# Optimization experiments

Hardware: AMD Instinct MI355X
Metric: run time of the kernel (lower is better)

Reference implementation:

```python
import math
import jax, jax.numpy as jnp
import numpy as np

B, S, D_MODEL, H = 2, 2048, 1024, 16
HD = D_MODEL // H  # head_dim = 64


def setup_inputs() -> dict:
    key = jax.random.key(0)
    ks = jax.random.split(key, 5)
    scale = 1.0 / math.sqrt(D_MODEL)
    return {
        "x": jax.random.normal(ks[0], (B, S, D_MODEL), dtype=jnp.float32),
        "attention_mask": jnp.ones((B, S), dtype=jnp.int32),
        "causal": 1,
        "Wq": jax.random.normal(ks[1], (D_MODEL, D_MODEL), dtype=jnp.float32) * scale,
        "Wk": jax.random.normal(ks[2], (D_MODEL, D_MODEL), dtype=jnp.float32) * scale,
        "Wv": jax.random.normal(ks[3], (D_MODEL, D_MODEL), dtype=jnp.float32) * scale,
        "Wo": jax.random.normal(ks[4], (D_MODEL, D_MODEL), dtype=jnp.float32) * scale,
    }


def reference(x, attention_mask, causal, Wq, Wk, Wv, Wo):
    b, s, d = x.shape
    # QKV projections, split heads -> (b, h, s, hd)
    q = (x @ Wq).reshape(b, s, H, HD).transpose(0, 2, 1, 3)
    k = (x @ Wk).reshape(b, s, H, HD).transpose(0, 2, 1, 3)
    v = (x @ Wv).reshape(b, s, H, HD).transpose(0, 2, 1, 3)

    score = jnp.einsum("bhqd,bhkd->bhqk", q, k) / math.sqrt(HD)

    neg_inf = jnp.float32(-jnp.inf)
    if causal:
        causal_mask = jnp.tril(jnp.ones((s, s), dtype=bool))  # (s, s)
        score = jnp.where(causal_mask[None, None, :, :], score, neg_inf)
    key_mask = attention_mask.astype(bool)[:, None, None, :]  # (b,1,1,s)
    score = jnp.where(key_mask, score, neg_inf)

    attn = jax.nn.softmax(score, axis=-1)  # numerically stable (max-subtracted)
    out = jnp.einsum("bhqk,bhkd->bhqd", attn, v)  # (b,h,s,hd)
    out = out.transpose(0, 2, 1, 3).reshape(b, s, d)
    return out @ Wo
```

## Files before the change

kernel.cpp:

```cpp
#include <hip/hip_runtime.h>
#include <hip/hip_bf16.h>

#define B_  2
#define S_  2048
#define D_  1024
#define H_  16
#define HD_ 64
#define BS_ (B_*S_)

typedef __attribute__((ext_vector_type(8))) short bf16x8;
typedef __attribute__((ext_vector_type(4))) float f32x4;
typedef __attribute__((ext_vector_type(4))) float float4v;
typedef __attribute__((ext_vector_type(4))) unsigned short ushort4v;
typedef __attribute__((ext_vector_type(2))) unsigned int uint2v;

__device__ __forceinline__ unsigned short f2bf(float f) {
  union { float f; unsigned int u; } v; v.f = f;
  unsigned int u = v.u;
  return (unsigned short)((u + 0x7fffu + ((u >> 16) & 1u)) >> 16);
}
__device__ __forceinline__ float bf2f(unsigned short u) {
  union { unsigned int i; float f; } v; v.i = ((unsigned int)u) << 16; return v.f;
}
__device__ __forceinline__ unsigned int cvtpk(float lo, float hi) {
  unsigned int r;
  asm("v_cvt_pk_bf16_f32 %0, %1, %2" : "=v"(r) : "v"(lo), "v"(hi));
  return r;
}

__device__ __forceinline__ void plswap16(float& a, float& b) {
#if __has_builtin(__builtin_amdgcn_permlane16_swap)
  uint2v r = __builtin_amdgcn_permlane16_swap(__float_as_uint(a), __float_as_uint(b), false, false);
  a = __uint_as_float(r[0]); b = __uint_as_float(r[1]);
#else
  asm volatile("v_permlane16_swap_b32 %0, %1" : "+v"(a), "+v"(b));
#endif
}
__device__ __forceinline__ void plswap32(float& a, float& b) {
#if __has_builtin(__builtin_amdgcn_permlane32_swap)
  uint2v r = __builtin_amdgcn_permlane32_swap(__float_as_uint(a), __float_as_uint(b), false, false);
  a = __uint_as_float(r[0]); b = __uint_as_float(r[1]);
#else
  asm volatile("v_permlane32_swap_b32 %0, %1" : "+v"(a), "+v"(b));
#endif
}
__device__ __forceinline__ float wave_max_lg(float x) {
  float t;
  asm volatile("v_mov_b32 %0, %1" : "=v"(t) : "v"(x));
  plswap16(x, t); x = fmaxf(x, t);
  asm volatile("v_mov_b32 %0, %1" : "=v"(t) : "v"(x));
  plswap32(x, t); x = fmaxf(x, t);
  return x;
}
__device__ __forceinline__ float wave_sum_lg(float x) {
  float t;
  asm volatile("v_mov_b32 %0, %1" : "=v"(t) : "v"(x));
  plswap16(x, t); x += t;
  asm volatile("v_mov_b32 %0, %1" : "=v"(t) : "v"(x));
  plswap32(x, t); x += t;
  return x;
}

__device__ __forceinline__ void gload16(const void* g, void* l) {
  __builtin_amdgcn_global_load_lds((const __attribute__((address_space(1))) void*)g,
                                   (__attribute__((address_space(3))) void*)l, 16, 0, 0);
}

__device__ __forceinline__ f32x4 mfma16(bf16x8 a, bf16x8 b, f32x4 c) {
  return __builtin_amdgcn_mfma_f32_16x16x32_bf16(a, b, c, 0, 0, 0);
}

__global__ __launch_bounds__(256) void k_prep(const float* __restrict__ x, unsigned short* __restrict__ xb,
                                              const float* __restrict__ w0, const float* __restrict__ w1,
                                              const float* __restrict__ w2, const float* __restrict__ w3,
                                              unsigned short* __restrict__ o0, unsigned short* __restrict__ o1,
                                              unsigned short* __restrict__ o2, unsigned short* __restrict__ o3) {
  const int bid = blockIdx.x;
  if (bid < 2048) {
    int i = bid * 256 + threadIdx.x;
    float4v a = ((const float4v*)x)[2*i];
    float4v b = ((const float4v*)x)[2*i + 1];
    union { bf16x8 v; unsigned short u[8]; } o;
#pragma unroll
    for (int j = 0; j < 4; ++j) { o.u[j] = f2bf(a[j]); o.u[4+j] = f2bf(b[j]); }
    ((bf16x8*)xb)[i] = o.v;
    return;
  }
  const int wid = bid - 2048;
  const int xx = wid & 15, yy = (wid >> 4) & 15, zz = wid >> 8;
  const float* w = zz == 0 ? w0 : zz == 1 ? w1 : zz == 2 ? w2 : w3;
  unsigned short* o = zz == 0 ? o0 : zz == 1 ? o1 : zz == 2 ? o2 : o3;
  __shared__ unsigned short til[64][68];
  const int n0 = xx * 64, k0 = yy * 64;
  const int t = threadIdx.x, r = t >> 4, c4 = t & 15;
#pragma unroll
  for (int i = 0; i < 4; ++i) {
    float4v v = *(const float4v*)(w + (size_t)(k0 + i*16 + r) * D_ + n0 + c4*4);
#pragma unroll
    for (int j = 0; j < 4; ++j) til[i*16 + r][c4*4 + j] = f2bf(v[j]);
  }
  __syncthreads();
#pragma unroll
  for (int i = 0; i < 4; ++i) {
    ushort4v u;
#pragma unroll
    for (int j = 0; j < 4; ++j) u[j] = til[c4*4 + j][i*16 + r];
    *(ushort4v*)(o + (size_t)(n0 + i*16 + r) * D_ + k0 + c4*4) = u;
  }
}

template <int MODE, typename OutT>
__device__ __forceinline__ void gemm_body(const unsigned short* __restrict__ A,
                                          const unsigned short* __restrict__ Bt,
                                          OutT* __restrict__ C,
                                          int M, int N, int K, int mblk, int nblk) {
  __shared__ unsigned short As[128 * 64];
  __shared__ unsigned short Bs[128 * 64];
  const int tid = threadIdx.x;
  const int w = tid >> 6, lane = tid & 63;
  const int lg = lane >> 4, li = lane & 15;
  const int m0 = mblk * 128, n0 = nblk * 128;
  const int wr = (w >> 1) * 64, wc = (w & 1) * 64;
  f32x4 acc[4][4] = {};
  for (int kt = 0; kt < K; kt += 64) {
#pragma unroll
    for (int i = 0; i < 4; ++i) {
      int c = (i*4 + w) * 64 + lane;
      int r = c >> 3, kc = c & 7;
      int off = ((kc ^ (r & 7)) << 3);
      gload16(A  + (size_t)(m0 + r) * K + kt + off, (char*)As + (i*4 + w) * 1024);
      gload16(Bt + (size_t)(n0 + r) * K + kt + off, (char*)Bs + (i*4 + w) * 1024);
    }
    __syncthreads();
#pragma unroll
    for (int ks = 0; ks < 2; ++ks) {
      bf16x8 af[4], bfr[4];
#pragma unroll
      for (int m = 0; m < 4; ++m) {
        int rr = wr + m*16 + li;
        int ch = (ks*4 + lg) ^ (rr & 7);
        af[m] = *(const bf16x8*)((const char*)As + rr*128 + ch*16);
      }
#pragma unroll
      for (int n = 0; n < 4; ++n) {
        int rr = wc + n*16 + li;
        int ch = (ks*4 + lg) ^ (rr & 7);
        bfr[n] = *(const bf16x8*)((const char*)Bs + rr*128 + ch*16);
      }
#pragma unroll
      for (int m = 0; m < 4; ++m)
#pragma unroll
        for (int n = 0; n < 4; ++n)
          acc[m][n] = mfma16(af[m], bfr[n], acc[m][n]);
    }
    __syncthreads();
  }
#pragma unroll
  for (int m = 0; m < 4; ++m)
#pragma unroll
    for (int n = 0; n < 4; ++n) {
      if (MODE == 2) {
        int gr = m0 + wr + m*16 + lg*4;
        int gc = n0 + wc + n*16 + li;
        int bb = gr >> 11, ss = gr & 2047, hh = gc >> 6, dd = gc & 63;
        unsigned short* p = (unsigned short*)C + ((size_t)((bb*H_ + hh)*HD_ + dd)) * S_ + ss;
        uint2v o2;
        o2[0] = cvtpk(acc[m][n][0], acc[m][n][1]);
        o2[1] = cvtpk(acc[m][n][2], acc[m][n][3]);
        *(uint2v*)p = o2;
      } else {
#pragma unroll
        for (int j = 0; j < 4; ++j) {
          int row = m0 + wr + m*16 + lg*4 + j;
          int col = n0 + wc + n*16 + li;
          if (MODE == 1) ((float*)C)[(size_t)row * N + col] = acc[m][n][j];
          else ((unsigned short*)C)[(size_t)row * N + col] = f2bf(acc[m][n][j]);
        }
      }
    }
}

__global__ __launch_bounds__(256, 2) void k_qkv(const unsigned short* __restrict__ xb,
    const unsigned short* __restrict__ wqt, const unsigned short* __restrict__ wkt,
    const unsigned short* __restrict__ wvt,
    unsigned short* __restrict__ Qb, unsigned short* __restrict__ Kb, unsigned short* __restrict__ Vtb) {
  const int z = blockIdx.z;
  if (z == 2) {
    gemm_body<2, unsigned short>(xb, wvt, Vtb, BS_, D_, D_, blockIdx.x, blockIdx.y);
  } else {
    gemm_body<0, unsigned short>(xb, z ? wkt : wqt, z ? Kb : Qb, BS_, D_, D_, blockIdx.x, blockIdx.y);
  }
}

__global__ __launch_bounds__(256, 2) void k_out(const unsigned short* __restrict__ AO,
                                                const unsigned short* __restrict__ wot,
                                                float* __restrict__ out) {
  gemm_body<1, float>(AO, wot, out, BS_, D_, D_, blockIdx.x, blockIdx.y);
}

__global__ __launch_bounds__(128, 2) void k_attn(const unsigned short* __restrict__ Q,
                                                 const unsigned short* __restrict__ K,
                                                 const unsigned short* __restrict__ Vt,
                                                 unsigned short* __restrict__ AO) {
  __shared__ unsigned short Ks[2 * 64 * 64];
  __shared__ unsigned short Vs[2 * 64 * 64];
  __shared__ unsigned short Ps[2 * 16 * 64];
  const int bh = blockIdx.x;
  const int qb = 63 - blockIdx.y;
  const int nkt = (qb >> 1) + 1;
  const int b = bh >> 4, h = bh & 15;
  const int tid = threadIdx.x, w = tid >> 6, lane = tid & 63;
  const int lg = lane >> 4, li = lane & 15;
  unsigned short* Psw = Ps + w * 1024;
  const float SC2 = 0.18033688f;

  const int qglob = qb*32 + w*16 + li;
  const unsigned short* qptr = Q + (size_t)(b*S_ + qglob) * D_ + h*HD_;
  union { bf16x8 v; unsigned short u[8]; } q0u, q1u;
  q0u.v = *(const bf16x8*)(qptr + lg*8);
  q1u.v = *(const bf16x8*)(qptr + 32 + lg*8);
#pragma unroll
  for (int j = 0; j < 8; ++j) {
    q0u.u[j] = f2bf(bf2f(q0u.u[j]) * SC2);
    q1u.u[j] = f2bf(bf2f(q1u.u[j]) * SC2);
  }
  const bf16x8 qf0 = q0u.v, qf1 = q1u.v;

  int paddr[8];
#pragma unroll
  for (int kj = 0; kj < 4; ++kj)
#pragma unroll
    for (int hh = 0; hh < 2; ++hh)
      paddr[kj*2 + hh] = li*128 + (((2*kj + (lg >> 1)) ^ (li & 7)) << 4) + (lg & 1)*8 + 4*hh;
  int pboff[2];
#pragma unroll
  for (int ks = 0; ks < 2; ++ks)
    pboff[ks] = li*128 + (((ks*4 + lg) ^ (li & 7)) << 4);

  int kofs[4], vofs[4];
#pragma unroll
  for (int i = 0; i < 4; ++i) {
    int c = i*128 + tid;
    int r = c >> 3, kc = c & 7;
    int off = ((kc ^ (r & 7)) << 3);
    kofs[i] = r * D_ + off;
    vofs[i] = r * S_ + off;
  }
  const unsigned short* kg = K  + (size_t)(b*S_) * D_ + h*HD_;
  const unsigned short* vg = Vt + (size_t)bh * HD_ * S_;

  f32x4 oacc[4] = {};
  float mrow = -1e30f, lrow = 0.f;

  auto stage = [&](int bsel, const unsigned short* kp, const unsigned short* vp) {
    char* KsB = (char*)Ks + bsel * 8192;
    char* VsB = (char*)Vs + bsel * 8192;
#pragma unroll
    for (int i = 0; i < 4; ++i) {
      gload16(kp + kofs[i], KsB + (i*2 + w) * 1024);
      gload16(vp + vofs[i], VsB + (i*2 + w) * 1024);
    }
  };

  stage(0, kg, vg);
  __syncthreads();

  for (int kt = 0; kt < nkt; ++kt) {
    const int cur = kt & 1;
    if (kt + 1 < nkt) {
      kg += 64 * D_; vg += 64;
      stage(cur ^ 1, kg, vg);
    }
    const char* KsB = (const char*)Ks + cur * 8192;
    const char* VsB = (const char*)Vs + cur * 8192;

    f32x4 sc[4];
    __builtin_amdgcn_s_setprio(1);
#pragma unroll
    for (int kj = 0; kj < 4; ++kj) {
      f32x4 t = {};
      t = mfma16(*(const bf16x8*)(KsB + kj*2048 + pboff[0]), qf0, t);
      t = mfma16(*(const bf16x8*)(KsB + kj*2048 + pboff[1]), qf1, t);
      sc[kj] = t;
    }
    __builtin_amdgcn_s_setprio(0);

    if (kt == nkt - 1) {
      const int qrel = qglob - kt*64;
#pragma unroll
      for (int kj = 0; kj < 4; ++kj)
#pragma unroll
        for (int j = 0; j < 4; ++j)
          if (kj*16 + lg*4 + j > qrel) sc[kj][j] = -1e30f;
    }

    float mx = sc[0][0];
#pragma unroll
    for (int kj = 0; kj < 4; ++kj)
#pragma unroll
      for (int j = 0; j < 4; ++j) mx = fmaxf(mx, sc[kj][j]);
    mx = wave_max_lg(mx);
    if (__any(mx > mrow + 8.f)) {
      const float mnew = fmaxf(mrow, mx);
      const float alpha = exp2f(mrow - mnew);
#pragma unroll
      for (int n = 0; n < 4; ++n)
#pragma unroll
        for (int j = 0; j < 4; ++j) oacc[n][j] *= alpha;
      lrow *= alpha;
      mrow = mnew;
    }
    f32x4 pv[4];
    float rs = 0.f;
#pragma unroll
    for (int kj = 0; kj < 4; ++kj)
#pragma unroll
      for (int j = 0; j < 4; ++j) {
        float p = exp2f(sc[kj][j] - mrow);
        rs += p;
        pv[kj][j] = p;
      }
    lrow += rs;

#pragma unroll
    for (int kj = 0; kj < 4; ++kj) {
      *(unsigned int*)((char*)Psw + paddr[kj*2 + 0]) = cvtpk(pv[kj][0], pv[kj][1]);
      *(unsigned int*)((char*)Psw + paddr[kj*2 + 1]) = cvtpk(pv[kj][2], pv[kj][3]);
    }

    const bf16x8 pf0 = *(const bf16x8*)((const char*)Psw + pboff[0]);
    const bf16x8 pf1 = *(const bf16x8*)((const char*)Psw + pboff[1]);
    __builtin_amdgcn_s_setprio(1);
#pragma unroll
    for (int n = 0; n < 4; ++n) {
      int vr = n*16 + li;
      int ch0 = lg ^ (vr & 7), ch1 = (4 + lg) ^ (vr & 7);
      oacc[n] = mfma16(*(const bf16x8*)(VsB + vr*128 + ch0*16), pf0, oacc[n]);
      oacc[n] = mfma16(*(const bf16x8*)(VsB + vr*128 + ch1*16), pf1, oacc[n]);
    }
    __builtin_amdgcn_s_setprio(0);
    __syncthreads();
  }

  lrow = wave_sum_lg(lrow);
  const float inv = 1.0f / lrow;
  unsigned short* aorow = AO + (size_t)(b*S_ + qglob) * D_ + h*HD_;
#pragma unroll
  for (int n = 0; n < 4; ++n) {
    uint2v o2;
    o2[0] = cvtpk(oacc[n][0] * inv, oacc[n][1] * inv);
    o2[1] = cvtpk(oacc[n][2] * inv, oacc[n][3] * inv);
    *(uint2v*)(aorow + n*16 + lg*4) = o2;
  }
}

extern "C" void kernel_launch(void* const* d_in, const int* in_sizes, int n_in,
                              void* d_out, int out_size, void* d_ws, size_t ws_size,
                              hipStream_t stream) {
  const float* x  = (const float*)d_in[0];
  const float* Wq = (const float*)d_in[3];
  const float* Wk = (const float*)d_in[4];
  const float* Wv = (const float*)d_in[5];
  const float* Wo = (const float*)d_in[6];
  float* out = (float*)d_out;

  unsigned short* ws  = (unsigned short*)d_ws;
  unsigned short* xb  = ws;
  unsigned short* wqt = xb  + (size_t)BS_ * D_;
  unsigned short* wkt = wqt + (size_t)D_ * D_;
  unsigned short* wvt = wkt + (size_t)D_ * D_;
  unsigned short* wot = wvt + (size_t)D_ * D_;
  unsigned short* Qb  = wot + (size_t)D_ * D_;
  unsigned short* Kb  = Qb  + (size_t)BS_ * D_;
  unsigned short* Vtb = Kb  + (size_t)BS_ * D_;
  unsigned short* AO  = Vtb + (size_t)BS_ * D_;

  k_prep<<<3072, 256, 0, stream>>>(x, xb, Wq, Wk, Wv, Wo, wqt, wkt, wvt, wot);
  k_qkv<<<dim3(32, 8, 3), 256, 0, stream>>>(xb, wqt, wkt, wvt, Qb, Kb, Vtb);
  k_attn<<<dim3(32, 64), 128, 0, stream>>>(Qb, Kb, Vtb, AO);
  k_out<<<dim3(32, 8), 256, 0, stream>>>(AO, wot, out);
}
```

Before: 117.9 us.

## Split long causal attention query blocks across two KV halves with combine kernel

Attention blocks now cover 64 query rows with 4 waves (256 threads), and the 16 longest query blocks per head are split into two KV-range chunks whose partial outputs and max/sum stats go to scratch buffers that reuse the xb/weight workspace. A new combine kernel merges the two partials with a log-sum-exp rescale. A constant lookup table orders the work longest-first to balance the causal load. The cost is an extra launch, extra global traffic for partials, and a combine kernel containing redundant leftover code.

```diff
diff --git a/kernel.cpp b/kernel.cpp
--- a/kernel.cpp
+++ b/kernel.cpp
@@ -13,6 +13,13 @@
 typedef __attribute__((ext_vector_type(4))) float float4v;
 typedef __attribute__((ext_vector_type(4))) unsigned short ushort4v;
 typedef __attribute__((ext_vector_type(2))) unsigned int uint2v;
+
+__constant__ unsigned char TQ[48] = {31,31,30,15, 30,29,29,28,14, 28,27,27,26,13,
+                                     26,25,25,24,12, 24,23,23,22,11, 22,21,21,20,10,
+                                     20,19,19,18,9, 18,17,17,16,8, 16,7, 6,5,4,3,2,1,0};
+__constant__ unsigned char TH[48] = {0,1,1,2, 0,0,1,1,2, 0,0,1,1,2,
+                                     0,0,1,1,2, 0,0,1,1,2, 0,0,1,1,2,
+                                     0,0,1,1,2, 0,0,1,1,2, 0,2, 2,2,2,2,2,2,2};
 
 __device__ __forceinline__ unsigned short f2bf(float f) {
   union { float f; unsigned int u; } v; v.f = f;
@@ -198,23 +205,29 @@
   gemm_body<1, float>(AO, wot, out, BS_, D_, D_, blockIdx.x, blockIdx.y);
 }
 
-__global__ __launch_bounds__(128, 2) void k_attn(const unsigned short* __restrict__ Q,
+__global__ __launch_bounds__(256, 4) void k_attn(const unsigned short* __restrict__ Q,
                                                  const unsigned short* __restrict__ K,
                                                  const unsigned short* __restrict__ Vt,
-                                                 unsigned short* __restrict__ AO) {
+                                                 unsigned short* __restrict__ AO,
+                                                 unsigned short* __restrict__ Opart,
+                                                 float* __restrict__ ML) {
   __shared__ unsigned short Ks[2 * 64 * 64];
   __shared__ unsigned short Vs[2 * 64 * 64];
-  __shared__ unsigned short Ps[2 * 16 * 64];
+  __shared__ unsigned short Ps[4 * 16 * 64];
   const int bh = blockIdx.x;
-  const int qb = 63 - blockIdx.y;
-  const int nkt = (qb >> 1) + 1;
+  const int y = blockIdx.y;
+  const int qb = TQ[y], ch = TH[y];
+  const int n = qb + 1, ka = n >> 1;
+  const int kt0 = (ch == 1) ? ka : 0;
+  const int kt1 = (ch == 0) ? ka : n;
+  const bool split = (ch != 2);
   const int b = bh >> 4, h = bh & 15;
   const int tid = threadIdx.x, w = tid >> 6, lane = tid & 63;
   const int lg = lane >> 4, li = lane & 15;
   unsigned short* Psw = Ps + w * 1024;
   const float SC2 = 0.18033688f;
 
-  const int qglob = qb*32 + w*16 + li;
+  const int qglob = qb*64 + w*16 + li;
   const unsigned short* qptr = Q + (size_t)(b*S_ + qglob) * D_ + h*HD_;
   union { bf16x8 v; unsigned short u[8]; } q0u, q1u;
   q0u.v = *(const bf16x8*)(qptr + lg*8);
@@ -237,17 +250,18 @@
   for (int ks = 0; ks < 2; ++ks)
     pboff[ks] = li*128 + (((ks*4 + lg) ^ (li & 7)) << 4);
 
-  int kofs[4], vofs[4];
-#pragma unroll
-  for (int i = 0; i < 4; ++i) {
-    int c = i*128 + tid;
+  int kofs[2], vofs[2], lofs[2];
+#pragma unroll
+  for (int i = 0; i < 2; ++i) {
+    int c = (i*4 + w) * 64 + lane;
     int r = c >> 3, kc = c & 7;
     int off = ((kc ^ (r & 7)) << 3);
     kofs[i] = r * D_ + off;
     vofs[i] = r * S_ + off;
-  }
-  const unsigned short* kg = K  + (size_t)(b*S_) * D_ + h*HD_;
-  const unsigned short* vg = Vt + (size_t)bh * HD_ * S_;
+    lofs[i] = (i*4 + w) * 1024;
+  }
+  const unsigned short* kg = K  + (size_t)(b*S_ + kt0*64) * D_ + h*HD_;
+  const unsigned short* vg = Vt + (size_t)bh * HD_ * S_ + kt0*64;
 
   f32x4 oacc[4] = {};
   float mrow = -1e30f, lrow = 0.f;
@@ -256,18 +270,18 @@
     char* KsB = (char*)Ks + bsel * 8192;
     char* VsB = (char*)Vs + bsel * 8192;
 #pragma unroll
-    for (int i = 0; i < 4; ++i) {
-      gload16(kp + kofs[i], KsB + (i*2 + w) * 1024);
-      gload16(vp + vofs[i], VsB + (i*2 + w) * 1024);
+    for (int i = 0; i < 2; ++i) {
+      gload16(kp + kofs[i], KsB + lofs[i]);
+      gload16(vp + vofs[i], VsB + lofs[i]);
     }
   };
 
   stage(0, kg, vg);
   __syncthreads();
 
-  for (int kt = 0; kt < nkt; ++kt) {
-    const int cur = kt & 1;
-    if (kt + 1 < nkt) {
+  for (int kt = kt0; kt < kt1; ++kt) {
+    const int cur = (kt - kt0) & 1;
+    if (kt + 1 < kt1) {
       kg += 64 * D_; vg += 64;
       stage(cur ^ 1, kg, vg);
     }
@@ -285,13 +299,13 @@
     }
     __builtin_amdgcn_s_setprio(0);
 
-    if (kt == nkt - 1) {
-      const int qrel = qglob - kt*64;
+    if (kt == qb) {
+      const int qloc = w*16 + li;
 #pragma unroll
       for (int kj = 0; kj < 4; ++kj)
 #pragma unroll
         for (int j = 0; j < 4; ++j)
-          if (kj*16 + lg*4 + j > qrel) sc[kj][j] = -1e30f;
+          if (kj*16 + lg*4 + j > qloc) sc[kj][j] = -1e30f;
     }
 
     float mx = sc[0][0];
@@ -304,13 +318,13 @@
       const float mnew = fmaxf(mrow, mx);
       const float alpha = exp2f(mrow - mnew);
 #pragma unroll
-      for (int n = 0; n < 4; ++n)
-#pragma unroll
-        for (int j = 0; j < 4; ++j) oacc[n][j] *= alpha;
+      for (int nn = 0; nn < 4; ++nn)
+#pragma unroll
+        for (int j = 0; j < 4; ++j) oacc[nn][j] *= alpha;
       lrow *= alpha;
       mrow = mnew;
     }
-    f32x4 pv[4];
+    f32x4 pvv[4];
     float rs = 0.f;
 #pragma unroll
     for (int kj = 0; kj < 4; ++kj)
@@ -318,40 +332,105 @@
       for (int j = 0; j < 4; ++j) {
         float p = exp2f(sc[kj][j] - mrow);
         rs += p;
-        pv[kj][j] = p;
+        pvv[kj][j] = p;
       }
     lrow += rs;
 
 #pragma unroll
     for (int kj = 0; kj < 4; ++kj) {
-      *(unsigned int*)((char*)Psw + paddr[kj*2 + 0]) = cvtpk(pv[kj][0], pv[kj][1]);
-      *(unsigned int*)((char*)Psw + paddr[kj*2 + 1]) = cvtpk(pv[kj][2], pv[kj][3]);
+      *(unsigned int*)((char*)Psw + paddr[kj*2 + 0]) = cvtpk(pvv[kj][0], pvv[kj][1]);
+      *(unsigned int*)((char*)Psw + paddr[kj*2 + 1]) = cvtpk(pvv[kj][2], pvv[kj][3]);
     }
 
     const bf16x8 pf0 = *(const bf16x8*)((const char*)Psw + pboff[0]);
     const bf16x8 pf1 = *(const bf16x8*)((const char*)Psw + pboff[1]);
     __builtin_amdgcn_s_setprio(1);
 #pragma unroll
-    for (int n = 0; n < 4; ++n) {
-      int vr = n*16 + li;
+    for (int nn = 0; nn < 4; ++nn) {
+      int vr = nn*16 + li;
       int ch0 = lg ^ (vr & 7), ch1 = (4 + lg) ^ (vr & 7);
-      oacc[n] = mfma16(*(const bf16x8*)(VsB + vr*128 + ch0*16), pf0, oacc[n]);
-      oacc[n] = mfma16(*(const bf16x8*)(VsB + vr*128 + ch1*16), pf1, oacc[n]);
+      oacc[nn] = mfma16(*(const bf16x8*)(VsB + vr*128 + ch0*16), pf0, oacc[nn]);
+      oacc[nn] = mfma16(*(const bf16x8*)(VsB + vr*128 + ch1*16), pf1, oacc[nn]);
     }
     __builtin_amdgcn_s_setprio(0);
     __syncthreads();
   }
 
   lrow = wave_sum_lg(lrow);
-  const float inv = 1.0f / lrow;
-  unsigned short* aorow = AO + (size_t)(b*S_ + qglob) * D_ + h*HD_;
-#pragma unroll
-  for (int n = 0; n < 4; ++n) {
-    uint2v o2;
-    o2[0] = cvtpk(oacc[n][0] * inv, oacc[n][1] * inv);
-    o2[1] = cvtpk(oacc[n][2] * inv, oacc[n][3] * inv);
-    *(uint2v*)(aorow + n*16 + lg*4) = o2;
-  }
+  if (!split) {
+    const float inv = 1.0f / lrow;
+    unsigned short* aorow = AO + (size_t)(b*S_ + qglob) * D_ + h*HD_;
+#pragma unroll
+    for (int nn = 0; nn < 4; ++nn) {
+      uint2v o2;
+      o2[0] = cvtpk(oacc[nn][0] * inv, oacc[nn][1] * inv);
+      o2[1] = cvtpk(oacc[nn][2] * inv, oacc[nn][3] * inv);
+      *(uint2v*)(aorow + nn*16 + lg*4) = o2;
+    }
+  } else {
+    const int slot = ((bh << 4) + (qb - 16)) * 2 + ch;
+    unsigned short* ob = Opart + (size_t)slot * 4096 + (w*16 + li) * 64;
+#pragma unroll
+    for (int nn = 0; nn < 4; ++nn) {
+      uint2v o2;
+      o2[0] = cvtpk(oacc[nn][0], oacc[nn][1]);
+      o2[1] = cvtpk(oacc[nn][2], oacc[nn][3]);
+      *(uint2v*)(ob + nn*16 + lg*4) = o2;
+    }
+    if (lg == 0) {
+      ML[slot*128 + (w*16 + li)]      = mrow;
+      ML[slot*128 + 64 + (w*16 + li)] = lrow;
+    }
+  }
+}
+
+__global__ __launch_bounds__(256) void k_comb(const unsigned short* __restrict__ Opart,
+                                              const float* __restrict__ ML,
+                                              unsigned short* __restrict__ AO) {
+  const int qx = blockIdx.x;
+  const int bh = blockIdx.y;
+  const int b = bh >> 4, h = bh & 15;
+  const int slot0 = ((bh << 4) + qx) * 2;
+  const int tid = threadIdx.x;
+  const int q = tid >> 2, dg = (tid & 3) * 16;
+  const float m0 = ML[slot0*128 + q],       l0 = ML[slot0*128 + 64 + q];
+  const float m1 = ML[(slot0+1)*128 + q],   l1 = ML[(slot0+1)*128 + 64 + q];
+  const float m = fmaxf(m0, m1);
+  float a0 = exp2f(m0 - m), a1 = exp2f(m1 - m);
+  const float inv = 1.0f / (l0*a0 + l1*a1);
+  a0 *= inv; a1 *= inv;
+  const unsigned short* o0 = Opart + (size_t)slot0 * 4096 + q*64 + dg;
+  const unsigned short* o1 = o0 + 4096;
+  union { bf16x8 v; unsigned short u[8]; } x0a, x0b, x1a, x1b;
+  x0a.v = *(const bf16x8*)o0;  x0b.v = *(const bf16x8*)(o0 + 8);
+  x1a.v = *(const bf16x8*)o1;  x1b.v = *(const bf16x8*)(o1 + 8);
+  unsigned short* ao = AO + (size_t)(b*S_ + (16 + qx)*64 + q) * D_ + h*HD_ + dg;
+  uint2v w0, w1;
+#pragma unroll
+  for (int j = 0; j < 4; ++j) {
+    float ea = bf2f(x0a.u[2*j])   * a0 + bf2f(x1a.u[2*j])   * a1;
+    float eb = bf2f(x0a.u[2*j+1]) * a0 + bf2f(x1a.u[2*j+1]) * a1;
+    float ec = bf2f(x0b.u[2*j])   * a0 + bf2f(x1b.u[2*j])   * a1;
+    float ed = bf2f(x0b.u[2*j+1]) * a0 + bf2f(x1b.u[2*j+1]) * a1;
+    if (j < 2) { w0[j] = cvtpk(ea, eb); } else { w0[j] = w0[j]; }
+    if (j < 2) w0[j] = cvtpk(ea, eb); else w1[j-2] = cvtpk(ea, eb);
+    if (j < 2) w1[j] = 0;
+    (void)ec; (void)ed;
+  }
+  w0[0] = cvtpk(bf2f(x0a.u[0])*a0 + bf2f(x1a.u[0])*a1, bf2f(x0a.u[1])*a0 + bf2f(x1a.u[1])*a1);
+  w0[1] = cvtpk(bf2f(x0a.u[2])*a0 + bf2f(x1a.u[2])*a1, bf2f(x0a.u[3])*a0 + bf2f(x1a.u[3])*a1);
+  uint2v w0b;
+  w0b[0] = cvtpk(bf2f(x0a.u[4])*a0 + bf2f(x1a.u[4])*a1, bf2f(x0a.u[5])*a0 + bf2f(x1a.u[5])*a1);
+  w0b[1] = cvtpk(bf2f(x0a.u[6])*a0 + bf2f(x1a.u[6])*a1, bf2f(x0a.u[7])*a0 + bf2f(x1a.u[7])*a1);
+  uint2v w1a, w1b;
+  w1a[0] = cvtpk(bf2f(x0b.u[0])*a0 + bf2f(x1b.u[0])*a1, bf2f(x0b.u[1])*a0 + bf2f(x1b.u[1])*a1);
+  w1a[1] = cvtpk(bf2f(x0b.u[2])*a0 + bf2f(x1b.u[2])*a1, bf2f(x0b.u[3])*a0 + bf2f(x1b.u[3])*a1);
+  w1b[0] = cvtpk(bf2f(x0b.u[4])*a0 + bf2f(x1b.u[4])*a1, bf2f(x0b.u[5])*a0 + bf2f(x1b.u[5])*a1);
+  w1b[1] = cvtpk(bf2f(x0b.u[6])*a0 + bf2f(x1b.u[6])*a1, bf2f(x0b.u[7])*a0 + bf2f(x1b.u[7])*a1);
+  *(uint2v*)(ao)      = w0;
+  *(uint2v*)(ao + 4)  = w0b;
+  *(uint2v*)(ao + 8)  = w1a;
+  *(uint2v*)(ao + 12) = w1b;
 }
 
 extern "C" void kernel_launch(void* const* d_in, const int* in_sizes, int n_in,
@@ -374,9 +453,12 @@
   unsigned short* Kb  = Qb  + (size_t)BS_ * D_;
   unsigned short* Vtb = Kb  + (size_t)BS_ * D_;
   unsigned short* AO  = Vtb + (size_t)BS_ * D_;
+  unsigned short* Opart = xb;
+  float* ML = (float*)wqt;
 
   k_prep<<<3072, 256, 0, stream>>>(x, xb, Wq, Wk, Wv, Wo, wqt, wkt, wvt, wot);
   k_qkv<<<dim3(32, 8, 3), 256, 0, stream>>>(xb, wqt, wkt, wvt, Qb, Kb, Vtb);
-  k_attn<<<dim3(32, 64), 128, 0, stream>>>(Qb, Kb, Vtb, AO);
+  k_attn<<<dim3(32, 48), 256, 0, stream>>>(Qb, Kb, Vtb, AO, Opart, ML);
+  k_comb<<<dim3(16, 32), 256, 0, stream>>>(Opart, ML, AO);
   k_out<<<dim3(32, 8), 256, 0, stream>>>(AO, wot, out);
 }
```

Measured after the change: 113.0 us. -4.2%, faster.
